# Kernel optimization log

Hardware: AMD Instinct MI355X
Metric: run time of the kernel (lower is better)

The kernel has to match this reference:

```python
import jax, jax.numpy as jnp
import numpy as np

N_NODES = 100000
N_EDGES = 3200000
IN_CH = 768
OUT_CH = 64
NEG_SLOPE = 0.2  # GATv2 default leaky_relu negative_slope


def setup_inputs() -> dict:
    key = jax.random.key(0)
    ks = jax.random.split(key, 9)
    node = jax.random.normal(ks[0], (N_NODES, IN_CH), dtype=jnp.float32)
    edge_index = jax.random.randint(ks[1], (2, N_EDGES), 0, N_NODES, dtype=jnp.int64)
    s = 0.02
    return {
        "node": node,
        "edge_index": edge_index,
        # GATv2Conv params (heads=1, share_weights=False)
        "W_l": jax.random.normal(ks[2], (IN_CH, OUT_CH), dtype=jnp.float32) * s,
        "b_l": jnp.zeros((OUT_CH,), dtype=jnp.float32),
        "W_r": jax.random.normal(ks[3], (IN_CH, OUT_CH), dtype=jnp.float32) * s,
        "b_r": jnp.zeros((OUT_CH,), dtype=jnp.float32),
        "att": jax.random.normal(ks[4], (OUT_CH,), dtype=jnp.float32) * s,
        "gnn_bias": jnp.zeros((OUT_CH,), dtype=jnp.float32),
        # parallel Linear branch
        "W_lin": jax.random.normal(ks[5], (IN_CH, OUT_CH), dtype=jnp.float32) * s,
        "b_lin": jnp.zeros((OUT_CH,), dtype=jnp.float32),
    }


def reference(node, edge_index, W_l, b_l, W_r, b_r, att, gnn_bias, W_lin, b_lin):
    N = node.shape[0]
    # add self loops
    loops = jnp.arange(N, dtype=edge_index.dtype)
    src = jnp.concatenate([edge_index[0], loops])  # message source j
    dst = jnp.concatenate([edge_index[1], loops])  # aggregation target i

    x_l = node @ W_l + b_l  # [N, C] source transform
    x_r = node @ W_r + b_r  # [N, C] target transform

    # GATv2 edge scores: a^T LeakyReLU(x_l[j] + x_r[i])
    e = jax.nn.leaky_relu(x_l[src] + x_r[dst], NEG_SLOPE) @ att  # [E]

    # segment softmax over edges grouped by destination
    m = jax.ops.segment_max(e, dst, num_segments=N)  # self loops -> no empty segments
    p = jnp.exp(e - m[dst])
    denom = jax.ops.segment_sum(p, dst, num_segments=N)
    alpha = p / denom[dst]  # [E]

    # weighted scatter-add aggregation of source messages
    out = jax.ops.segment_sum(alpha[:, None] * x_l[src], dst, num_segments=N)
    out = out + gnn_bias

    # parallel linear branch + ReLU (dropout = identity in eval mode)
    out = out + node @ W_lin + b_lin
    return jax.nn.relu(out)
```

## Files before the change

### kernel.cpp

```cpp
#include <hip/hip_runtime.h>
#include <hip/hip_bf16.h>

#define NN 100000
#define NE 3200000
#define KD 768

#define BW 128
#define NBUK 782
#define CAPB 4608
#define CHUNK 8192

typedef __bf16 bf16;
typedef __bf16 bf16x8 __attribute__((ext_vector_type(8)));
typedef float f32x4 __attribute__((ext_vector_type(4)));

__global__ void k_detect(const int* __restrict__ ei, int* __restrict__ meta) {
    if (blockIdx.x == 0 && threadIdx.x == 0) {
        int odd_or = 0;
        for (int t = 0; t < 16; ++t) odd_or |= ei[2 * t + 1];
        meta[0] = (odd_or == 0) ? 2 : 1;
    }
}

__global__ void k_trans(const float* __restrict__ Wl, const float* __restrict__ Wr,
                        const float* __restrict__ Wlin, bf16* __restrict__ BT) {
    int t = blockIdx.x * 256 + threadIdx.x;
    if (t >= 192 * KD) return;
    int n = t / KD, k = t % KD;
    const float* W = (n < 64) ? Wl : (n < 128) ? Wr : Wlin;
    BT[t] = (bf16)W[k * 64 + (n & 63)];
}

__device__ __forceinline__ bf16x8 cvt8(float4 a, float4 b) {
    bf16x8 r;
    r[0] = (bf16)a.x; r[1] = (bf16)a.y; r[2] = (bf16)a.z; r[3] = (bf16)a.w;
    r[4] = (bf16)b.x; r[5] = (bf16)b.y; r[6] = (bf16)b.z; r[7] = (bf16)b.w;
    return r;
}

__global__ __launch_bounds__(256, 4) void k_gemm(
    const float* __restrict__ node, const bf16* __restrict__ BT,
    const float* __restrict__ bl, const float* __restrict__ br,
    const float* __restrict__ blin, const float* __restrict__ gbias,
    bf16* __restrict__ xl, bf16* __restrict__ xr, float* __restrict__ base) {
    int wave = threadIdx.x >> 6, lane = threadIdx.x & 63;
    int quad = lane >> 4, l16 = lane & 15;
    int r0 = blockIdx.x * 64 + (wave & 1) * 32;
    int c0 = (wave >> 1) * 96;

    f32x4 acc[2][6] = {};
    long a0 = (long)((r0 + l16 < NN) ? r0 + l16 : NN - 1) * KD;
    long a1 = (long)((r0 + 16 + l16 < NN) ? r0 + 16 + l16 : NN - 1) * KD;
    int kq = quad * 8;

    float4 c00 = *(const float4*)(node + a0 + kq);
    float4 c01 = *(const float4*)(node + a0 + kq + 4);
    float4 c10 = *(const float4*)(node + a1 + kq);
    float4 c11 = *(const float4*)(node + a1 + kq + 4);

    for (int kt = 0; kt < KD; kt += 32) {
        int kkn = ((kt + 32 < KD) ? kt + 32 : 0) + kq;
        float4 n00 = *(const float4*)(node + a0 + kkn);
        float4 n01 = *(const float4*)(node + a0 + kkn + 4);
        float4 n10 = *(const float4*)(node + a1 + kkn);
        float4 n11 = *(const float4*)(node + a1 + kkn + 4);

        bf16x8 af0 = cvt8(c00, c01);
        bf16x8 af1 = cvt8(c10, c11);
        int kk = kt + kq;
        const bf16* bp = BT + (size_t)(c0 + l16) * KD + kk;
#pragma unroll
        for (int nf = 0; nf < 6; ++nf) {
            bf16x8 bfr = *(const bf16x8*)(bp + (size_t)nf * 16 * KD);
            acc[0][nf] = __builtin_amdgcn_mfma_f32_16x16x32_bf16(af0, bfr, acc[0][nf], 0, 0, 0);
            acc[1][nf] = __builtin_amdgcn_mfma_f32_16x16x32_bf16(af1, bfr, acc[1][nf], 0, 0, 0);
        }
        c00 = n00; c01 = n01; c10 = n10; c11 = n11;
    }
#pragma unroll
    for (int rf = 0; rf < 2; ++rf)
#pragma unroll
        for (int nf = 0; nf < 6; ++nf)
#pragma unroll
            for (int i = 0; i < 4; ++i) {
                int row = r0 + rf * 16 + quad * 4 + i;
                int gcol = c0 + nf * 16 + l16;
                if (row >= NN) continue;
                float v = acc[rf][nf][i];
                if (gcol < 64) {
                    xl[row * 64 + gcol] = (bf16)(v + bl[gcol]);
                } else if (gcol < 128) {
                    int c = gcol - 64;
                    xr[row * 64 + c] = (bf16)(v + br[c]);
                } else {
                    int c = gcol - 128;
                    base[row * 64 + c] = v + blin[c] + gbias[c];
                }
            }
}

__global__ __launch_bounds__(1024) void k_bucket(
    const int* __restrict__ ei, const int* __restrict__ meta,
    int* __restrict__ gcnt, int* __restrict__ gstore) {
    __shared__ int hist[NBUK], excl[NBUK], lcur[NBUK], gbase[NBUK];
    __shared__ int sorted[CHUNK];
    __shared__ int wsum[16], wexcl[17];
    int tid = threadIdx.x, wv = tid >> 6, ln = tid & 63;
    long e0 = (long)blockIdx.x * CHUNK;
    int nedge = (int)(((long)NE - e0) < CHUNK ? ((long)NE - e0) : CHUNK);
    int st = meta[0];

    for (int k = tid; k < NBUK; k += 1024) hist[k] = 0;
    __syncthreads();
    for (int k = tid; k < nedge; k += 1024) {
        int d = ei[(size_t)NE * st + (size_t)(e0 + k) * st];
        atomicAdd(&hist[d >> 7], 1);
    }
    __syncthreads();
    {
        int v = (tid < NBUK) ? hist[tid] : 0;
        int s = v;
#pragma unroll
        for (int off = 1; off < 64; off <<= 1) {
            int t = __shfl_up(s, off, 64);
            if (ln >= off) s += t;
        }
        if (ln == 63) wsum[wv] = s;
        __syncthreads();
        if (wv == 0 && ln < 16) {
            int ws = wsum[ln];
#pragma unroll
            for (int off = 1; off < 16; off <<= 1) {
                int t = __shfl_up(ws, off, 64);
                if (ln >= off) ws += t;
            }
            wexcl[ln + 1] = ws;
            if (ln == 0) wexcl[0] = 0;
        }
        __syncthreads();
        if (tid < NBUK) {
            int ex = wexcl[wv] + s - v;
            excl[tid] = ex;
            lcur[tid] = ex;
        }
    }
    for (int k = tid; k < NBUK; k += 1024) {
        int c = hist[k];
        gbase[k] = c ? atomicAdd(&gcnt[k], c) : 0;
    }
    __syncthreads();
    for (int k = tid; k < nedge; k += 1024) {
        int s = ei[(size_t)(e0 + k) * st];
        int d = ei[(size_t)NE * st + (size_t)(e0 + k) * st];
        int pos = atomicAdd(&lcur[d >> 7], 1);
        sorted[pos] = (s << 7) | (d & 127);
    }
    __syncthreads();
    for (int b = wv; b < NBUK; b += 16) {
        int cnt = hist[b], lo = excl[b], gb = gbase[b];
        for (int k = ln; k < cnt; k += 64) {
            int gp = gb + k;
            if (gp < CAPB) gstore[(size_t)b * CAPB + gp] = sorted[lo + k];
        }
    }
}

__global__ __launch_bounds__(1024) void k_agg2(
    const bf16* __restrict__ xl, const bf16* __restrict__ xr,
    const float* __restrict__ att, const int* __restrict__ gcnt,
    const int* __restrict__ gstore, float* __restrict__ out) {
    __shared__ int raw[CAPB], srt[CAPB];
    __shared__ int rp[BW + 1], cur[BW], h[BW];
    int b = blockIdx.x, tid = threadIdx.x;
    int len = gcnt[b]; if (len > CAPB) len = CAPB;

    if (tid < BW) h[tid] = 0;
    __syncthreads();
    for (int k = tid; k < len; k += 1024) {
        int p = gstore[(size_t)b * CAPB + k];
        raw[k] = p;
        atomicAdd(&h[p & 127], 1);
    }
    __syncthreads();
    if (tid < 64) {
        int a0 = h[tid], a1 = h[64 + tid];
        int s0 = a0, s1 = a1;
#pragma unroll
        for (int off = 1; off < 64; off <<= 1) {
            int t0 = __shfl_up(s0, off, 64);
            int t1 = __shfl_up(s1, off, 64);
            if (tid >= off) { s0 += t0; s1 += t1; }
        }
        int tot0 = __shfl(s0, 63, 64);
        rp[tid + 1] = s0;
        rp[65 + tid] = s1 + tot0;
        if (tid == 0) rp[0] = 0;
    }
    __syncthreads();
    if (tid < BW) cur[tid] = rp[tid];
    __syncthreads();
    for (int k = tid; k < len; k += 1024) {
        int p = raw[k];
        int pos = atomicAdd(&cur[p & 127], 1);
        srt[pos] = p >> 7;
    }
    __syncthreads();

    int wv = tid >> 6, lane = tid & 63;
    int quad = lane >> 4, l16 = lane & 15;
    float att_c = att[lane];
    bf16x8 b_lo, b_hi;
#pragma unroll
    for (int j = 0; j < 8; ++j) {
        b_lo[j] = (bf16)att[quad * 8 + j];
        b_hi[j] = (bf16)att[32 + quad * 8 + j];
    }
    for (int dl = wv; dl < BW; dl += 16) {
        int i = b * BW + dl;
        if (i >= NN) break;
        float xr_c = (float)xr[(size_t)i * 64 + lane];
        float xl_c = (float)xl[(size_t)i * 64 + lane];
        bf16x8 xr_lo = *(const bf16x8*)(xr + (size_t)i * 64 + quad * 8);
        bf16x8 xr_hi = *(const bf16x8*)(xr + (size_t)i * 64 + 32 + quad * 8);

        float s = xl_c + xr_c;
        float v = att_c * (s > 0.f ? s : 0.2f * s);
#pragma unroll
        for (int m = 32; m; m >>= 1) v += __shfl_xor(v, m, 64);
        float p0 = __expf(v);
        float denom = p0;
        float accv = p0 * xl_c;

        int beg = rp[dl], end = rp[dl + 1];
        for (int eb = beg; eb < end; eb += 16) {
            int idx = eb + l16;
            int jc = srt[(idx < end) ? idx : beg];
            bf16x8 a_lo = *(const bf16x8*)(xl + (size_t)jc * 64 + quad * 8);
            bf16x8 a_hi = *(const bf16x8*)(xl + (size_t)jc * 64 + 32 + quad * 8);
            bf16x8 f_lo, f_hi;
#pragma unroll
            for (int j = 0; j < 8; ++j) {
                float a = (float)a_lo[j] + (float)xr_lo[j];
                f_lo[j] = (bf16)(a > 0.f ? a : 0.2f * a);
                float b2 = (float)a_hi[j] + (float)xr_hi[j];
                f_hi[j] = (bf16)(b2 > 0.f ? b2 : 0.2f * b2);
            }
            f32x4 sc = {0.f, 0.f, 0.f, 0.f};
            sc = __builtin_amdgcn_mfma_f32_16x16x32_bf16(f_lo, b_lo, sc, 0, 0, 0);
            sc = __builtin_amdgcn_mfma_f32_16x16x32_bf16(f_hi, b_hi, sc, 0, 0, 0);
            float p[4];
#pragma unroll
            for (int r = 0; r < 4; ++r) {
                float pe = __expf(sc[r]);
                p[r] = (eb + quad * 4 + r < end) ? pe : 0.f;
            }
#pragma unroll
            for (int t = 0; t < 16; ++t) {
                float pt = __shfl(p[t & 3], (t >> 2) * 16, 64);
                int jj = __shfl(jc, t, 64);
                float xlv = (float)xl[(size_t)jj * 64 + lane];
                denom += pt;
                accv += pt * xlv;
            }
        }
        float o = accv / denom + out[(size_t)i * 64 + lane];
        out[(size_t)i * 64 + lane] = (o > 0.f ? o : 0.f);
    }
}

extern "C" void kernel_launch(void* const* d_in, const int* in_sizes, int n_in,
                              void* d_out, int out_size, void* d_ws, size_t ws_size,
                              hipStream_t stream) {
    const float* node = (const float*)d_in[0];
    const int* ei     = (const int*)d_in[1];
    const float* Wl   = (const float*)d_in[2];
    const float* bl   = (const float*)d_in[3];
    const float* Wr   = (const float*)d_in[4];
    const float* br   = (const float*)d_in[5];
    const float* attv = (const float*)d_in[6];
    const float* gb   = (const float*)d_in[7];
    const float* Wlin = (const float*)d_in[8];
    const float* blin = (const float*)d_in[9];
    float* out = (float*)d_out;

    char* w = (char*)d_ws;
    bf16* xl    = (bf16*)w;   w += (size_t)NN * 64 * 2;
    bf16* xr    = (bf16*)w;   w += (size_t)NN * 64 * 2;
    bf16* BT    = (bf16*)w;   w += (size_t)192 * KD * 2;
    int* meta   = (int*)w;    w += 64;
    int* gcnt   = (int*)w;    w += (size_t)NBUK * 4 + 64;
    int* gstore = (int*)w;    w += (size_t)NBUK * CAPB * 4;

    hipMemsetAsync(gcnt, 0, (size_t)NBUK * 4, stream);
    k_detect<<<1, 64, 0, stream>>>(ei, meta);
    k_trans<<<(192 * KD + 255) / 256, 256, 0, stream>>>(Wl, Wr, Wlin, BT);
    k_gemm<<<(NN + 63) / 64, 256, 0, stream>>>(node, BT, bl, br, blin, gb, xl, xr, out);
    k_bucket<<<(NE + CHUNK - 1) / CHUNK, 1024, 0, stream>>>(ei, meta, gcnt, gstore);
    k_agg2<<<NBUK, 1024, 0, stream>>>(xl, xr, attv, gcnt, gstore, out);
}
```

Measured before the change: 810.6 us.

## Stage GEMM A tiles through LDS with async global_load_lds double buffering

The projection GEMM used to load the fp32 node rows straight into registers, so every wave pair sharing a row block loaded the same A data. Now each 64x32 fp32 A tile is fetched once per block into a double-buffered, XOR-swizzled LDS tile using global_load_lds, and waves read their fragments from LDS. This removes the duplicate global reads of A and overlaps the next tile's load with the current MFMAs. The cost is two block-wide barriers per k-step and extra LDS use, which may hurt occupancy.

```diff
diff --git a/kernel.cpp b/kernel.cpp
--- a/kernel.cpp
+++ b/kernel.cpp
@@ -13,6 +13,11 @@
 typedef __bf16 bf16;
 typedef __bf16 bf16x8 __attribute__((ext_vector_type(8)));
 typedef float f32x4 __attribute__((ext_vector_type(4)));
+
+#define GLD16(g, l)                                                          \
+    __builtin_amdgcn_global_load_lds(                                        \
+        (const __attribute__((address_space(1))) void*)(g),                  \
+        (__attribute__((address_space(3))) void*)(l), 16, 0, 0)
 
 __global__ void k_detect(const int* __restrict__ ei, int* __restrict__ meta) {
     if (blockIdx.x == 0 && threadIdx.x == 0) {
@@ -43,39 +48,50 @@
     const float* __restrict__ bl, const float* __restrict__ br,
     const float* __restrict__ blin, const float* __restrict__ gbias,
     bf16* __restrict__ xl, bf16* __restrict__ xr, float* __restrict__ base) {
-    int wave = threadIdx.x >> 6, lane = threadIdx.x & 63;
+    __shared__ float As[2][64 * 32];
+    int tid = threadIdx.x;
+    int wave = tid >> 6, lane = tid & 63;
     int quad = lane >> 4, l16 = lane & 15;
-    int r0 = blockIdx.x * 64 + (wave & 1) * 32;
+    int rblk = blockIdx.x * 64;
     int c0 = (wave >> 1) * 96;
+    int rlo = (wave & 1) * 32 + l16;
+    int rhi = rlo + 16;
+
+    int row_a = tid >> 3, slot_a = tid & 7;
+    int row_b = row_a + 32;
+    long ga = (long)((rblk + row_a < NN) ? rblk + row_a : NN - 1) * KD
+              + ((slot_a ^ (row_a & 7)) << 2);
+    long gb = (long)((rblk + row_b < NN) ? rblk + row_b : NN - 1) * KD
+              + ((slot_a ^ (row_b & 7)) << 2);
 
     f32x4 acc[2][6] = {};
-    long a0 = (long)((r0 + l16 < NN) ? r0 + l16 : NN - 1) * KD;
-    long a1 = (long)((r0 + 16 + l16 < NN) ? r0 + 16 + l16 : NN - 1) * KD;
-    int kq = quad * 8;
-
-    float4 c00 = *(const float4*)(node + a0 + kq);
-    float4 c01 = *(const float4*)(node + a0 + kq + 4);
-    float4 c10 = *(const float4*)(node + a1 + kq);
-    float4 c11 = *(const float4*)(node + a1 + kq + 4);
-
+
+    GLD16(node + ga, &As[0][tid * 4]);
+    GLD16(node + gb, &As[0][1024 + tid * 4]);
+
+    int buf = 0;
     for (int kt = 0; kt < KD; kt += 32) {
-        int kkn = ((kt + 32 < KD) ? kt + 32 : 0) + kq;
-        float4 n00 = *(const float4*)(node + a0 + kkn);
-        float4 n01 = *(const float4*)(node + a0 + kkn + 4);
-        float4 n10 = *(const float4*)(node + a1 + kkn);
-        float4 n11 = *(const float4*)(node + a1 + kkn + 4);
-
-        bf16x8 af0 = cvt8(c00, c01);
-        bf16x8 af1 = cvt8(c10, c11);
-        int kk = kt + kq;
-        const bf16* bp = BT + (size_t)(c0 + l16) * KD + kk;
+        __syncthreads();
+        if (kt + 32 < KD) {
+            GLD16(node + ga + kt + 32, &As[buf ^ 1][tid * 4]);
+            GLD16(node + gb + kt + 32, &As[buf ^ 1][1024 + tid * 4]);
+        }
+        int cA = 2 * quad, cB = 2 * quad + 1;
+        float4 lo0 = *(const float4*)&As[buf][rlo * 32 + ((cA ^ (rlo & 7)) << 2)];
+        float4 lo1 = *(const float4*)&As[buf][rlo * 32 + ((cB ^ (rlo & 7)) << 2)];
+        float4 hi0 = *(const float4*)&As[buf][rhi * 32 + ((cA ^ (rhi & 7)) << 2)];
+        float4 hi1 = *(const float4*)&As[buf][rhi * 32 + ((cB ^ (rhi & 7)) << 2)];
+        bf16x8 af0 = cvt8(lo0, lo1);
+        bf16x8 af1 = cvt8(hi0, hi1);
+        const bf16* bp = BT + (size_t)(c0 + l16) * KD + kt + quad * 8;
 #pragma unroll
         for (int nf = 0; nf < 6; ++nf) {
             bf16x8 bfr = *(const bf16x8*)(bp + (size_t)nf * 16 * KD);
             acc[0][nf] = __builtin_amdgcn_mfma_f32_16x16x32_bf16(af0, bfr, acc[0][nf], 0, 0, 0);
             acc[1][nf] = __builtin_amdgcn_mfma_f32_16x16x32_bf16(af1, bfr, acc[1][nf], 0, 0, 0);
         }
-        c00 = n00; c01 = n01; c10 = n10; c11 = n11;
+        buf ^= 1;
+        __syncthreads();
     }
 #pragma unroll
     for (int rf = 0; rf < 2; ++rf)
@@ -83,7 +99,7 @@
         for (int nf = 0; nf < 6; ++nf)
 #pragma unroll
             for (int i = 0; i < 4; ++i) {
-                int row = r0 + rf * 16 + quad * 4 + i;
+                int row = rblk + (wave & 1) * 32 + rf * 16 + quad * 4 + i;
                 int gcol = c0 + nf * 16 + l16;
                 if (row >= NN) continue;
                 float v = acc[rf][nf][i];
```

Result: no change. 804.0 us (-0.8%).
